# Kernel optimization log

Hardware: AMD Instinct MI355X
Metric: run time of the kernel (lower is better)

Reference implementation:

```python
import jax, jax.numpy as jnp
import numpy as np

RES = (512, 512)
MAX_VAL = 100.0
OBJ_WIDTH = 5
N_ITERS = 5
SIGMA = 0.2


def setup_inputs() -> dict:
    key = jax.random.key(0)
    ks = jax.random.split(key, 6)
    H, W = RES
    x = jax.random.uniform(ks[0], (1, H, W, 2), jnp.float32) * 2.0 - 1.0  # query grid in [-1,1]
    boundary_types = jax.random.randint(ks[1], (H, W), 0, 2, jnp.int32)
    boundary_conditions = jax.random.uniform(ks[2], (H, W), jnp.float32)
    B_enc = SIGMA * jax.random.normal(ks[3], (64, 2), jnp.float32)  # GaussianEncoding(0.2, 2, 64)
    Wh = jax.random.normal(ks[4], (4, 128, 128), jnp.float32) / jnp.sqrt(128.0)
    W_out = jax.random.normal(ks[5], (128, 1), jnp.float32) / jnp.sqrt(128.0)
    return {"x": x, "boundary_types": boundary_types,
            "boundary_conditions": boundary_conditions,
            "B_enc": B_enc, "Wh": Wh, "W_out": W_out}


def _box_filter(a, width):
    # width x width mean filter, 'same' padding (F.conv2d with ones/width^2 kernel)
    k = jnp.ones((1, 1, width, width), a.dtype) / float(width * width)
    return jax.lax.conv_general_dilated(a[None, None], k, (1, 1), "SAME")[0, 0]


def _grid_sample_2d(img, grid):
    # img [H,W]; grid [N,2] with (x,y) in [-1,1]; bilinear, align_corners=True, border padding
    H, W = img.shape
    ix = jnp.clip((grid[:, 0] + 1.0) * 0.5 * (W - 1), 0.0, W - 1.0)
    iy = jnp.clip((grid[:, 1] + 1.0) * 0.5 * (H - 1), 0.0, H - 1.0)
    x0 = jnp.floor(ix).astype(jnp.int32)
    y0 = jnp.floor(iy).astype(jnp.int32)
    x1 = jnp.clip(x0 + 1, 0, W - 1)
    y1 = jnp.clip(y0 + 1, 0, H - 1)
    wx = ix - x0
    wy = iy - y0
    return (img[y0, x0] * (1 - wx) * (1 - wy) + img[y0, x1] * wx * (1 - wy)
            + img[y1, x0] * (1 - wx) * wy + img[y1, x1] * wx * wy)


def _solve(V0, C, boundary_types, boundary_conditions):
    # 5 Jacobi-style 8-neighbor stencil passes: free cells take the neighbor
    # average plus local cost; boundary cells are pinned to their conditions.
    free = boundary_types == 0

    def step(V, _):
        Vp = jnp.pad(V, 1, mode="edge")
        nb = (Vp[:-2, :-2] + Vp[:-2, 1:-1] + Vp[:-2, 2:]
              + Vp[1:-1, :-2] + Vp[1:-1, 2:]
              + Vp[2:, :-2] + Vp[2:, 1:-1] + Vp[2:, 2:]) / 8.0
        return jnp.where(free, nb + C, boundary_conditions), None

    V, _ = jax.lax.scan(step, V0, None, length=N_ITERS)
    return V


def reference(x, boundary_types, boundary_conditions, B_enc, Wh, W_out):
    H, W = RES
    free = boundary_types == 0
    # V init: max_val everywhere, boundary cells pinned (obj_inds = boundary_types > 0)
    V0 = jnp.where(free, jnp.float32(MAX_VAL), boundary_conditions)

    # Gaussian random Fourier feature encoding of 0.5 + 0.5*x -> 128 dims
    xq = 0.5 + 0.5 * x.reshape(-1, 2)
    vp = (2.0 * jnp.pi) * (xq @ B_enc.T)            # [N, 64]
    enc = jnp.concatenate([jnp.cos(vp), jnp.sin(vp)], axis=-1)  # [N, 128]

    # FullyFusedMLP: 4 hidden ReLU layers of 128 neurons, linear 1-dim output, no bias
    h = enc
    for i in range(Wh.shape[0]):
        h = jax.nn.relu(h @ Wh[i])
    C = (h @ W_out).reshape(H, W)
    C_pos = jax.nn.relu(C)

    # extra cost: box-filtered obstacle boundary values splashed onto free cells
    obj = boundary_conditions * (boundary_types == 1) * (boundary_conditions > 0)
    extra = _box_filter(obj, OBJ_WIDTH) * free
    Cs = C_pos + extra

    out_grid = _solve(V0, Cs, boundary_types, boundary_conditions)
    out = _grid_sample_2d(out_grid, x.reshape(-1, 2)).reshape(H, W)
    return out, C
```

## Files before the change

### kernel.cpp

```cpp
#include <hip/hip_runtime.h>


typedef unsigned short ushort_t;
typedef short short8 __attribute__((ext_vector_type(8)));
typedef float floatx4 __attribute__((ext_vector_type(4)));

#define HH 512
#define WW 512
#define NPIX (HH*WW)

#define SW(p, f) (((p) << 7) + (((((f) >> 3) ^ ((p) & 15))) << 3) + ((f) & 7))

__device__ inline ushort_t f2bf(float f) {
    union { float f; unsigned int i; } v; v.f = f;
    unsigned int u = v.i;
    unsigned int r = u + 0x7FFFu + ((u >> 16) & 1u);
    return (ushort_t)(r >> 16);
}
__device__ inline float bf2f(ushort_t u) {
    union { unsigned int i; float f; } v; v.i = ((unsigned int)u) << 16; return v.f;
}

__device__ inline void async_copy16(void* lds, const void* g) {
    __builtin_amdgcn_global_load_lds(
        (const __attribute__((address_space(1))) unsigned int*)g,
        (__attribute__((address_space(3))) unsigned int*)lds, 16, 0, 0);
}

__global__ void prep_kernel(const float* __restrict__ Wh,
                            uint4* __restrict__ WT) {
    int g = blockIdx.x * 256 + threadIdx.x;
    int pc = g & 15, n = (g >> 4) & 127, l = g >> 11;
    int c = pc ^ (n & 15);
    int k0 = c << 3;
    const float* src = Wh + l * 16384 + n;
    unsigned int w[4];
    #pragma unroll
    for (int j = 0; j < 4; ++j) {
        ushort_t a = f2bf(src[(k0 + 2 * j)     * 128]);
        ushort_t b = f2bf(src[(k0 + 2 * j + 1) * 128]);
        w[j] = (unsigned int)a | ((unsigned int)b << 16);
    }
    WT[g] = uint4{w[0], w[1], w[2], w[3]};
}

__global__ __launch_bounds__(256, 2) void mlp_kernel(const float* __restrict__ x,
                                                     const ushort_t* __restrict__ WT,
                                                     const float* __restrict__ benc,
                                                     const float* __restrict__ wout,
                                                     float* __restrict__ C_ws,
                                                     float* __restrict__ outbuf) {
    __shared__ __align__(16) ushort_t act[128 * 128];
    __shared__ __align__(16) ushort_t wbuf[128 * 128];
    const int tid = threadIdx.x;
    const int p0 = blockIdx.x * 128;
    const int lane = tid & 63, wave = tid >> 6;

    {
        const char* src = (const char*)WT;
        int base = wave * 512;
        #pragma unroll
        for (int c2 = 0; c2 < 8; ++c2) {
            int cb = base + c2 * 64;
            async_copy16(&wbuf[cb * 8], src + (cb + lane) * 16);
        }
    }

    {
        int p = tid >> 1, h = tid & 1;
        float2 xv = ((const float2*)x)[p0 + p];
        float xq0 = 0.5f + 0.5f * xv.x, xq1 = 0.5f + 0.5f * xv.y;
        const float4* b4 = (const float4*)benc;
        #pragma unroll 4
        for (int f2 = 0; f2 < 32; f2 += 2) {
            int f = h * 32 + f2;
            float4 b = b4[f >> 1];
            float vp0 = 6.28318530718f * (xq0 * b.x + xq1 * b.y);
            float vp1 = 6.28318530718f * (xq0 * b.z + xq1 * b.w);
            float s0, c0, s1, c1;
            __sincosf(vp0, &s0, &c0);
            __sincosf(vp1, &s1, &c1);
            unsigned int pc = (unsigned int)f2bf(c0) | ((unsigned int)f2bf(c1) << 16);
            unsigned int ps = (unsigned int)f2bf(s0) | ((unsigned int)f2bf(s1) << 16);
            *(unsigned int*)&act[SW(p, f)]      = pc;
            *(unsigned int*)&act[SW(p, f + 64)] = ps;
        }
    }

    const int quad = lane >> 4, l16 = lane & 15;
    const int ntb = (wave >> 1) * 64;
    const int ptb = (wave & 1) * 64;

    #pragma unroll 1
    for (int l = 0; l < 4; ++l) {
        __syncthreads();

        floatx4 acc[4][4];
        #pragma unroll
        for (int i = 0; i < 4; ++i)
            #pragma unroll
            for (int j = 0; j < 4; ++j)
                acc[i][j] = floatx4{0.0f, 0.0f, 0.0f, 0.0f};

        #pragma unroll
        for (int ks = 0; ks < 4; ++ks) {
            int cs = (ks * 4 + quad);
            short8 af[4], bv[4];
            #pragma unroll
            for (int i = 0; i < 4; ++i) {
                int r = ntb + i * 16 + l16;
                af[i] = *(const short8*)&wbuf[(r << 7) + ((cs ^ l16) << 3)];
            }
            #pragma unroll
            for (int j = 0; j < 4; ++j) {
                int p = ptb + j * 16 + l16;
                bv[j] = *(const short8*)&act[(p << 7) + ((cs ^ l16) << 3)];
            }
            #pragma unroll
            for (int i = 0; i < 4; ++i)
                #pragma unroll
                for (int j = 0; j < 4; ++j)
                    acc[i][j] = __builtin_amdgcn_mfma_f32_16x16x32_bf16(af[i], bv[j], acc[i][j], 0, 0, 0);
        }
        __syncthreads();

        if (l < 3) {
            const char* src = (const char*)WT + (l + 1) * 32768;
            int base = wave * 512;
            #pragma unroll
            for (int c2 = 0; c2 < 8; ++c2) {
                int cb = base + c2 * 64;
                async_copy16(&wbuf[cb * 8], src + (cb + lane) * 16);
            }
        }

        #pragma unroll
        for (int i = 0; i < 4; ++i) {
            #pragma unroll
            for (int j = 0; j < 4; ++j) {
                int p = ptb + j * 16 + l16;
                int n0 = ntb + i * 16 + quad * 4;
                float r0 = fmaxf(acc[i][j][0], 0.0f);
                float r1 = fmaxf(acc[i][j][1], 0.0f);
                float r2 = fmaxf(acc[i][j][2], 0.0f);
                float r3 = fmaxf(acc[i][j][3], 0.0f);
                uint2 pk;
                pk.x = (unsigned int)f2bf(r0) | ((unsigned int)f2bf(r1) << 16);
                pk.y = (unsigned int)f2bf(r2) | ((unsigned int)f2bf(r3) << 16);
                *(uint2*)&act[SW(p, n0)] = pk;
            }
        }
    }
    __syncthreads();

    {
        int p = tid >> 1, h = tid & 1;
        const float4* wo4 = (const float4*)wout;
        float sum = 0.0f;
        #pragma unroll
        for (int g = 0; g < 8; ++g) {
            int ch = h * 8 + g;
            short8 v = *(const short8*)&act[(p << 7) + ((ch ^ (p & 15)) << 3)];
            float4 wa = wo4[ch * 2], wb = wo4[ch * 2 + 1];
            sum += bf2f((ushort_t)v[0]) * wa.x + bf2f((ushort_t)v[1]) * wa.y
                 + bf2f((ushort_t)v[2]) * wa.z + bf2f((ushort_t)v[3]) * wa.w
                 + bf2f((ushort_t)v[4]) * wb.x + bf2f((ushort_t)v[5]) * wb.y
                 + bf2f((ushort_t)v[6]) * wb.z + bf2f((ushort_t)v[7]) * wb.w;
        }
        float other = __shfl_xor(sum, 1);
        if (h == 0) {
            float tot = sum + other;
            C_ws[p0 + p] = tot;
            outbuf[NPIX + p0 + p] = tot;
        }
    }
}

#define TS 48
__global__ __launch_bounds__(256) void fused_solve_kernel(const int* __restrict__ bt,
                                                          const float* __restrict__ bc,
                                                          const float* __restrict__ C_ws,
                                                          float* __restrict__ Vfin) {
    __shared__ float Va[46 * TS];
    __shared__ float Vb[46 * TS];
    __shared__ float Wp[46 * TS];
    const int tid = threadIdx.x;
    const int tx0 = (blockIdx.x & 15) * 32, ty0 = (blockIdx.x >> 4) * 32;
    const int gx0 = tx0 - 7, gy0 = ty0 - 7;

    for (int c = tid; c < 46 * 46; c += 256) {
        int li = c / 46, lj = c - li * 46;
        int gi = gy0 + li, gj = gx0 + lj;
        float v = 0.0f;
        if (gi >= 0 && gi < HH && gj >= 0 && gj < WW) {
            int g = gi * WW + gj;
            float b = bc[g];
            if (bt[g] == 1 && b > 0.0f) v = b;
        }
        Va[li * TS + lj] = v;
    }
    __syncthreads();

    for (int c = tid; c < 42 * 42; c += 256) {
        int li = 2 + c / 42, lj = 2 + c - (c / 42) * 42;
        int gi = gy0 + li, gj = gx0 + lj;
        float w = -1.0f, v0 = 0.0f;
        if (gi >= 0 && gi < HH && gj >= 0 && gj < WW) {
            int g = gi * WW + gj;
            if (bt[g] == 0) {
                float s = 0.0f;
                #pragma unroll
                for (int di = 0; di < 5; ++di)
                    #pragma unroll
                    for (int dj = 0; dj < 5; ++dj)
                        s += Va[(li + di - 2) * TS + lj + dj - 2];
                w = fmaxf(C_ws[g], 0.0f) + s * 0.04f;
                v0 = 100.0f;
            } else {
                float b = bc[g];
                w = -b - 1.0f;
                v0 = b;
            }
        }
        Wp[li * TS + lj] = w;
        Vb[li * TS + lj] = v0;
    }
    __syncthreads();

    float* src = Vb;
    float* dst = Va;
    #pragma unroll 1
    for (int t = 0; t < 5; ++t) {
        for (int c = tid; c < 42 * 42; c += 256) {
            int li = 2 + c / 42, lj = 2 + c - (c / 42) * 42;
            int gi = gy0 + li, gj = gx0 + lj;
            if (gi < 0 || gi >= HH || gj < 0 || gj >= WW) continue;
            float w = Wp[li * TS + lj];
            float v;
            if (w < 0.0f) {
                v = -w - 1.0f;
            } else {
                int um = (gi > 0)      ? li - 1 : li;
                int dp = (gi < HH - 1) ? li + 1 : li;
                int lm = (gj > 0)      ? lj - 1 : lj;
                int rp = (gj < WW - 1) ? lj + 1 : lj;
                float s = src[um * TS + lm] + src[um * TS + lj] + src[um * TS + rp]
                        + src[li * TS + lm]                     + src[li * TS + rp]
                        + src[dp * TS + lm] + src[dp * TS + lj] + src[dp * TS + rp];
                v = s * 0.125f + w;
            }
            dst[li * TS + lj] = v;
        }
        __syncthreads();
        float* tmp = src; src = dst; dst = tmp;
    }

    for (int c = tid; c < 1024; c += 256) {
        int li = 7 + (c >> 5), lj = 7 + (c & 31);
        Vfin[(gy0 + li) * WW + gx0 + lj] = src[li * TS + lj];
    }
}

__global__ void sample_kernel(const float* __restrict__ x,
                              const float* __restrict__ V,
                              float* __restrict__ out) {
    int idx = blockIdx.x * 256 + threadIdx.x;
    float2 g2 = ((const float2*)x)[idx];
    float ix = (g2.x + 1.0f) * 0.5f * 511.0f;
    float iy = (g2.y + 1.0f) * 0.5f * 511.0f;
    ix = fminf(fmaxf(ix, 0.0f), 511.0f);
    iy = fminf(fmaxf(iy, 0.0f), 511.0f);
    int x0 = (int)floorf(ix), y0 = (int)floorf(iy);
    int x1 = min(x0 + 1, 511), y1 = min(y0 + 1, 511);
    float wx = ix - (float)x0, wy = iy - (float)y0;
    float v00 = V[y0 * 512 + x0], v01 = V[y0 * 512 + x1];
    float v10 = V[y1 * 512 + x0], v11 = V[y1 * 512 + x1];
    float v = v00 * (1.0f - wx) * (1.0f - wy) + v01 * wx * (1.0f - wy)
            + v10 * (1.0f - wx) * wy          + v11 * wx * wy;
    out[idx] = v;
}

extern "C" void kernel_launch(void* const* d_in, const int* in_sizes, int n_in,
                              void* d_out, int out_size, void* d_ws, size_t ws_size,
                              hipStream_t stream) {
    const float* x    = (const float*)d_in[0];
    const int*   bt   = (const int*)d_in[1];
    const float* bc   = (const float*)d_in[2];
    const float* benc = (const float*)d_in[3];
    const float* Wh   = (const float*)d_in[4];
    const float* wout = (const float*)d_in[5];

    char* ws = (char*)d_ws;
    ushort_t* WT   = (ushort_t*)(ws + 4096);
    float*    C_ws = (float*)(ws + 262144);
    float*    Vfin = (float*)(ws + 262144 + 3 * (1 << 20));
    float*    outp = (float*)d_out;

    prep_kernel<<<32, 256, 0, stream>>>(Wh, (uint4*)WT);
    mlp_kernel<<<2048, 256, 0, stream>>>(x, WT, benc, wout, C_ws, outp);
    fused_solve_kernel<<<256, 256, 0, stream>>>(bt, bc, C_ws, Vfin);
    sample_kernel<<<1024, 256, 0, stream>>>(x, Vfin, outp);
}
```

Baseline: 144.7 us.

## Read MLP weights from global memory, shrink solve tiles, transpose weights via LDS

The MLP kernel drops its LDS weight buffer and async global-to-LDS copies. Each wave now loads weight fragments straight from global or L2 memory, which halves LDS use so occupancy can rise to 4 blocks per CU. The stencil solve kernel moves to 16x16 output tiles with a 32-wide padded layout and four times as many blocks, and prep_kernel now transposes through shared memory for coalesced access. In exchange, every block rereads the weights from cache instead of LDS, and the smaller solve tiles carry a larger share of redundant halo work.

```diff
diff --git a/kernel.cpp b/kernel.cpp
--- a/kernel.cpp
+++ b/kernel.cpp
@@ -21,50 +21,42 @@
     union { unsigned int i; float f; } v; v.i = ((unsigned int)u) << 16; return v.f;
 }
 
-__device__ inline void async_copy16(void* lds, const void* g) {
-    __builtin_amdgcn_global_load_lds(
-        (const __attribute__((address_space(1))) unsigned int*)g,
-        (__attribute__((address_space(3))) unsigned int*)lds, 16, 0, 0);
-}
-
-__global__ void prep_kernel(const float* __restrict__ Wh,
-                            uint4* __restrict__ WT) {
-    int g = blockIdx.x * 256 + threadIdx.x;
-    int pc = g & 15, n = (g >> 4) & 127, l = g >> 11;
-    int c = pc ^ (n & 15);
-    int k0 = c << 3;
-    const float* src = Wh + l * 16384 + n;
-    unsigned int w[4];
+__global__ __launch_bounds__(256) void prep_kernel(const float* __restrict__ Wh,
+                                                   ushort_t* __restrict__ WT) {
+    __shared__ float trans[64 * 33];
+    const int tid = threadIdx.x;
+    const int l = blockIdx.x >> 3, ng = (blockIdx.x >> 2) & 1, kq = blockIdx.x & 3;
+    const int n0 = ng * 64, k0 = kq * 32;
+    const int ln = tid & 63, wv = tid >> 6;
     #pragma unroll
-    for (int j = 0; j < 4; ++j) {
-        ushort_t a = f2bf(src[(k0 + 2 * j)     * 128]);
-        ushort_t b = f2bf(src[(k0 + 2 * j + 1) * 128]);
-        w[j] = (unsigned int)a | ((unsigned int)b << 16);
-    }
-    WT[g] = uint4{w[0], w[1], w[2], w[3]};
-}
-
-__global__ __launch_bounds__(256, 2) void mlp_kernel(const float* __restrict__ x,
+    for (int pass = 0; pass < 8; ++pass) {
+        int k = k0 + pass * 4 + wv;
+        trans[ln * 33 + (k - k0)] = Wh[l * 16384 + k * 128 + n0 + ln];
+    }
+    __syncthreads();
+    {
+        int n = tid >> 2, q = tid & 3;
+        unsigned int w[4];
+        #pragma unroll
+        for (int j = 0; j < 4; ++j) {
+            ushort_t a = f2bf(trans[n * 33 + q * 8 + 2 * j]);
+            ushort_t b = f2bf(trans[n * 33 + q * 8 + 2 * j + 1]);
+            w[j] = (unsigned int)a | ((unsigned int)b << 16);
+        }
+        *(uint4*)&WT[(l * 128 + n0 + n) * 128 + k0 + q * 8] = uint4{w[0], w[1], w[2], w[3]};
+    }
+}
+
+__global__ __launch_bounds__(256, 4) void mlp_kernel(const float* __restrict__ x,
                                                      const ushort_t* __restrict__ WT,
                                                      const float* __restrict__ benc,
                                                      const float* __restrict__ wout,
                                                      float* __restrict__ C_ws,
                                                      float* __restrict__ outbuf) {
     __shared__ __align__(16) ushort_t act[128 * 128];
-    __shared__ __align__(16) ushort_t wbuf[128 * 128];
     const int tid = threadIdx.x;
     const int p0 = blockIdx.x * 128;
     const int lane = tid & 63, wave = tid >> 6;
-
-    {
-        const char* src = (const char*)WT;
-        int base = wave * 512;
-        #pragma unroll
-        for (int c2 = 0; c2 < 8; ++c2) {
-            int cb = base + c2 * 64;
-            async_copy16(&wbuf[cb * 8], src + (cb + lane) * 16);
-        }
-    }
 
     {
         int p = tid >> 1, h = tid & 1;
@@ -77,9 +69,8 @@
             float4 b = b4[f >> 1];
             float vp0 = 6.28318530718f * (xq0 * b.x + xq1 * b.y);
             float vp1 = 6.28318530718f * (xq0 * b.z + xq1 * b.w);
-            float s0, c0, s1, c1;
-            __sincosf(vp0, &s0, &c0);
-            __sincosf(vp1, &s1, &c1);
+            float s0 = __sinf(vp0), c0 = __cosf(vp0);
+            float s1 = __sinf(vp1), c1 = __cosf(vp1);
             unsigned int pc = (unsigned int)f2bf(c0) | ((unsigned int)f2bf(c1) << 16);
             unsigned int ps = (unsigned int)f2bf(s0) | ((unsigned int)f2bf(s1) << 16);
             *(unsigned int*)&act[SW(p, f)]      = pc;
@@ -104,12 +95,12 @@
 
         #pragma unroll
         for (int ks = 0; ks < 4; ++ks) {
-            int cs = (ks * 4 + quad);
+            int cs = ks * 4 + quad;
             short8 af[4], bv[4];
             #pragma unroll
             for (int i = 0; i < 4; ++i) {
                 int r = ntb + i * 16 + l16;
-                af[i] = *(const short8*)&wbuf[(r << 7) + ((cs ^ l16) << 3)];
+                af[i] = *(const short8*)&WT[((l * 128 + r) << 7) + (cs << 3)];
             }
             #pragma unroll
             for (int j = 0; j < 4; ++j) {
@@ -123,16 +114,6 @@
                     acc[i][j] = __builtin_amdgcn_mfma_f32_16x16x32_bf16(af[i], bv[j], acc[i][j], 0, 0, 0);
         }
         __syncthreads();
-
-        if (l < 3) {
-            const char* src = (const char*)WT + (l + 1) * 32768;
-            int base = wave * 512;
-            #pragma unroll
-            for (int c2 = 0; c2 < 8; ++c2) {
-                int cb = base + c2 * 64;
-                async_copy16(&wbuf[cb * 8], src + (cb + lane) * 16);
-            }
-        }
 
         #pragma unroll
         for (int i = 0; i < 4; ++i) {
@@ -176,36 +157,35 @@
     }
 }
 
-#define TS 48
 __global__ __launch_bounds__(256) void fused_solve_kernel(const int* __restrict__ bt,
                                                           const float* __restrict__ bc,
                                                           const float* __restrict__ C_ws,
                                                           float* __restrict__ Vfin) {
-    __shared__ float Va[46 * TS];
-    __shared__ float Vb[46 * TS];
-    __shared__ float Wp[46 * TS];
+    __shared__ float Va[30 * 32];
+    __shared__ float Vb[30 * 32];
+    __shared__ float Wp[30 * 32];
     const int tid = threadIdx.x;
-    const int tx0 = (blockIdx.x & 15) * 32, ty0 = (blockIdx.x >> 4) * 32;
-    const int gx0 = tx0 - 7, gy0 = ty0 - 7;
-
-    for (int c = tid; c < 46 * 46; c += 256) {
-        int li = c / 46, lj = c - li * 46;
+    const int gx0 = (blockIdx.x & 31) * 16 - 7, gy0 = (blockIdx.x >> 5) * 16 - 7;
+
+    for (int c = tid; c < 30 * 32; c += 256) {
+        int li = c >> 5, lj = c & 31;
         int gi = gy0 + li, gj = gx0 + lj;
         float v = 0.0f;
-        if (gi >= 0 && gi < HH && gj >= 0 && gj < WW) {
+        if (lj < 30 && gi >= 0 && gi < HH && gj >= 0 && gj < WW) {
             int g = gi * WW + gj;
             float b = bc[g];
             if (bt[g] == 1 && b > 0.0f) v = b;
         }
-        Va[li * TS + lj] = v;
-    }
-    __syncthreads();
-
-    for (int c = tid; c < 42 * 42; c += 256) {
-        int li = 2 + c / 42, lj = 2 + c - (c / 42) * 42;
+        Va[c] = v;
+    }
+    __syncthreads();
+
+    for (int c = tid; c < 30 * 32; c += 256) {
+        int li = c >> 5, lj = c & 31;
         int gi = gy0 + li, gj = gx0 + lj;
         float w = -1.0f, v0 = 0.0f;
-        if (gi >= 0 && gi < HH && gj >= 0 && gj < WW) {
+        if (li >= 2 && li < 28 && lj >= 2 && lj < 28 &&
+            gi >= 0 && gi < HH && gj >= 0 && gj < WW) {
             int g = gi * WW + gj;
             if (bt[g] == 0) {
                 float s = 0.0f;
@@ -213,7 +193,7 @@
                 for (int di = 0; di < 5; ++di)
                     #pragma unroll
                     for (int dj = 0; dj < 5; ++dj)
-                        s += Va[(li + di - 2) * TS + lj + dj - 2];
+                        s += Va[(li + di - 2) * 32 + lj + dj - 2];
                 w = fmaxf(C_ws[g], 0.0f) + s * 0.04f;
                 v0 = 100.0f;
             } else {
@@ -222,8 +202,8 @@
                 v0 = b;
             }
         }
-        Wp[li * TS + lj] = w;
-        Vb[li * TS + lj] = v0;
+        Wp[c] = w;
+        Vb[c] = v0;
     }
     __syncthreads();
 
@@ -231,33 +211,33 @@
     float* dst = Va;
     #pragma unroll 1
     for (int t = 0; t < 5; ++t) {
-        for (int c = tid; c < 42 * 42; c += 256) {
-            int li = 2 + c / 42, lj = 2 + c - (c / 42) * 42;
-            int gi = gy0 + li, gj = gx0 + lj;
-            if (gi < 0 || gi >= HH || gj < 0 || gj >= WW) continue;
-            float w = Wp[li * TS + lj];
+        for (int c = tid; c < 26 * 32; c += 256) {
+            int li = 2 + (c >> 5), lj = c & 31;
+            if (lj < 2 || lj >= 28) continue;
+            float w = Wp[li * 32 + lj];
             float v;
             if (w < 0.0f) {
                 v = -w - 1.0f;
             } else {
+                int gi = gy0 + li, gj = gx0 + lj;
                 int um = (gi > 0)      ? li - 1 : li;
                 int dp = (gi < HH - 1) ? li + 1 : li;
                 int lm = (gj > 0)      ? lj - 1 : lj;
                 int rp = (gj < WW - 1) ? lj + 1 : lj;
-                float s = src[um * TS + lm] + src[um * TS + lj] + src[um * TS + rp]
-                        + src[li * TS + lm]                     + src[li * TS + rp]
-                        + src[dp * TS + lm] + src[dp * TS + lj] + src[dp * TS + rp];
+                float s = src[um * 32 + lm] + src[um * 32 + lj] + src[um * 32 + rp]
+                        + src[li * 32 + lm]                     + src[li * 32 + rp]
+                        + src[dp * 32 + lm] + src[dp * 32 + lj] + src[dp * 32 + rp];
                 v = s * 0.125f + w;
             }
-            dst[li * TS + lj] = v;
+            dst[li * 32 + lj] = v;
         }
         __syncthreads();
         float* tmp = src; src = dst; dst = tmp;
     }
 
-    for (int c = tid; c < 1024; c += 256) {
-        int li = 7 + (c >> 5), lj = 7 + (c & 31);
-        Vfin[(gy0 + li) * WW + gx0 + lj] = src[li * TS + lj];
+    {
+        int li = 7 + (tid >> 4), lj = 7 + (tid & 15);
+        Vfin[(gy0 + li) * WW + gx0 + lj] = src[li * 32 + lj];
     }
 }
 
@@ -296,8 +276,8 @@
     float*    Vfin = (float*)(ws + 262144 + 3 * (1 << 20));
     float*    outp = (float*)d_out;
 
-    prep_kernel<<<32, 256, 0, stream>>>(Wh, (uint4*)WT);
+    prep_kernel<<<32, 256, 0, stream>>>(Wh, WT);
     mlp_kernel<<<2048, 256, 0, stream>>>(x, WT, benc, wout, C_ws, outp);
-    fused_solve_kernel<<<256, 256, 0, stream>>>(bt, bc, C_ws, Vfin);
+    fused_solve_kernel<<<1024, 256, 0, stream>>>(bt, bc, C_ws, Vfin);
     sample_kernel<<<1024, 256, 0, stream>>>(x, Vfin, outp);
 }
```

Result: slower. 190.6 us (+31.7%).
